# Kernel optimization log

Hardware: AMD Instinct MI355X
Metric: run time of the kernel (lower is better)

Reference implementation:

```python
import jax, jax.numpy as jnp
import numpy as np

N = 100000
E = 3200000
F_IN = 256
D_OUT = 128


def setup_inputs() -> dict:
    key = jax.random.key(0)
    ks = jax.random.split(key, 12)
    x = jax.random.normal(ks[0], (N, F_IN), dtype=jnp.float32)
    adj_val = jax.random.uniform(ks[1], (E,), dtype=jnp.float32)
    edge_row = jnp.sort(jax.random.randint(ks[2], (E,), 0, N))
    edge_col = jax.random.randint(ks[3], (E,), 0, N)
    # learned params (glorot-ish scaling)
    W1 = jax.random.normal(ks[4], (F_IN, D_OUT), dtype=jnp.float32) * (1.0 / np.sqrt(F_IN))   # conv1d_1 (1x1, no bias)
    w2 = jax.random.normal(ks[5], (D_OUT, 1), dtype=jnp.float32) * (1.0 / np.sqrt(D_OUT))     # conv1d_2
    b2 = jnp.zeros((1,), dtype=jnp.float32)
    w3 = jax.random.normal(ks[6], (D_OUT, 1), dtype=jnp.float32) * (1.0 / np.sqrt(D_OUT))     # conv1d_3
    b3 = jnp.zeros((1,), dtype=jnp.float32)
    kernel = jax.random.normal(ks[7], (F_IN, D_OUT), dtype=jnp.float32) * (1.0 / np.sqrt(F_IN))
    bias = jax.random.normal(ks[8], (N, D_OUT), dtype=jnp.float32) * 0.02
    return {"x": x, "adj_val": adj_val, "W1": W1, "w2": w2, "b2": b2,
            "w3": w3, "b3": b3, "kernel": kernel, "bias": bias,
            "edge_row": edge_row, "edge_col": edge_col}


def reference(x, adj_val, W1, w2, b2, w3, b3, kernel, bias, edge_row, edge_col):
    # 1x1 conv projections (equivalent to per-node dense layers)
    mapped = x @ W1                                   # [N, D]
    sa1 = (mapped @ w2 + b2)[:, 0]                    # [N]
    sa2 = (mapped @ w3 + b3)[:, 0]                    # [N]
    # sparse*dense broadcast then sparse add: per edge (i,j):
    #   adj_val * sa1[i] + adj_val * sa2[j]
    e = adj_val * (sa1[edge_row] + sa2[edge_col])     # [E]
    e = jax.nn.leaky_relu(e, negative_slope=0.2)
    # sparse row-wise softmax over nonzero entries
    m = jax.ops.segment_max(e, edge_row, num_segments=N)        # [N]
    m = jnp.where(jnp.isfinite(m), m, 0.0)
    ex = jnp.exp(e - m[edge_row])                               # [E]
    denom = jax.ops.segment_sum(ex, edge_row, num_segments=N)   # [N]
    denom = jnp.where(denom > 0, denom, 1.0)
    att = ex / denom[edge_row]                                  # [E]
    # dense feature transform then SpMM aggregation
    value = x @ kernel                                          # [N, D_OUT]
    out = jax.ops.segment_sum(att[:, None] * value[edge_col], edge_row, num_segments=N)
    out = out + bias                                            # use_bias=True
    return out  # activation=None (linear), single head, 'average' reduction
```

## Files before the change

### kernel.cpp

```cpp
#include <hip/hip_runtime.h>
#include <math.h>

#define N_NODES 100000
#define N_EDGES 3200000
#define F_IN    256
#define D_OUT   128

typedef __attribute__((ext_vector_type(8))) short short8;
typedef __attribute__((ext_vector_type(4))) float f32x4;

__device__ __forceinline__ unsigned short f2bf(float f) {
    unsigned u = __float_as_uint(f);
    unsigned r = (u + 0x7FFFu + ((u >> 16) & 1u)) >> 16;
    return (unsigned short)r;
}

__device__ __forceinline__ float dot4(float4 a, float4 b) {
    return a.x * b.x + a.y * b.y + a.z * b.z + a.w * b.w;
}

__device__ __forceinline__ float sb(unsigned u, int k) {
    return (float)((int)(u << ((3 - k) * 8)) >> 24);
}

__global__ __launch_bounds__(128) void prep_kernel(
    const float* __restrict__ W1, const float* __restrict__ w2,
    const float* __restrict__ w3, const float* __restrict__ kern,
    float* __restrict__ v1, float* __restrict__ v2,
    unsigned short* __restrict__ kbT) {
    const int kk  = blockIdx.x;
    const int tid = threadIdx.x;
    kbT[(size_t)tid * F_IN + kk] = f2bf(kern[(size_t)kk * D_OUT + tid]);
    if (tid < 64) {
        const float* wr = W1 + (size_t)kk * D_OUT;
        float a = wr[tid], b = wr[tid + 64];
        float s1 = a * w2[tid] + b * w2[tid + 64];
        float s2 = a * w3[tid] + b * w3[tid + 64];
#pragma unroll
        for (int o = 32; o > 0; o >>= 1) {
            s1 += __shfl_xor(s1, o);
            s2 += __shfl_xor(s2, o);
        }
        if (tid == 0) { v1[kk] = s1; v2[kk] = s2; }
    }
}

__global__ void row_ptr_kernel(const int* __restrict__ edge_row,
                               int* __restrict__ row_ptr) {
    int r = blockIdx.x * blockDim.x + threadIdx.x;
    if (r > N_NODES) return;
    int lo = 0, hi = N_EDGES;
    while (lo < hi) {
        int mid = (lo + hi) >> 1;
        if (edge_row[mid] < r) lo = mid + 1; else hi = mid;
    }
    row_ptr[r] = lo;
}

__global__ __launch_bounds__(256) void gemm_sa_kernel(
    const float* __restrict__ x, const unsigned short* __restrict__ kbT,
    const float* __restrict__ v1, const float* __restrict__ v2,
    const float* __restrict__ b2p, const float* __restrict__ b3p,
    signed char* __restrict__ valq, float* __restrict__ scale,
    float* __restrict__ sa1, float* __restrict__ sa2) {
    const int wid = blockIdx.x * 4 + (threadIdx.x >> 6);
    const int m_base = wid * 32;
    if (m_base >= N_NODES) return;
    const int lane = threadIdx.x & 63;
    const int r = lane & 15;
    const int q = lane >> 4;

    const float4* x0 = (const float4*)(x + (size_t)(m_base + r) * F_IN + q * 8);
    const float4* x1 = (const float4*)(x + (size_t)(m_base + 16 + r) * F_IN + q * 8);

    f32x4 acc[2][8];
#pragma unroll
    for (int t = 0; t < 2; ++t)
#pragma unroll
        for (int nt = 0; nt < 8; ++nt) acc[t][nt] = (f32x4)(0.f);
    float s1a = 0.f, s1b = 0.f, s2a = 0.f, s2b = 0.f;

#pragma unroll 2
    for (int s = 0; s < 8; ++s) {
        float4 p00 = x0[s * 8];
        float4 p01 = x0[s * 8 + 1];
        float4 p10 = x1[s * 8];
        float4 p11 = x1[s * 8 + 1];
        const float4* vp1 = (const float4*)(v1 + s * 32 + q * 8);
        const float4* vp2 = (const float4*)(v2 + s * 32 + q * 8);
        float4 va = vp1[0], vb = vp1[1], vc = vp2[0], vd = vp2[1];
        s1a += dot4(p00, va) + dot4(p01, vb);
        s2a += dot4(p00, vc) + dot4(p01, vd);
        s1b += dot4(p10, va) + dot4(p11, vb);
        s2b += dot4(p10, vc) + dot4(p11, vd);

        short8 a0, a1;
        a0[0] = (short)f2bf(p00.x); a0[1] = (short)f2bf(p00.y);
        a0[2] = (short)f2bf(p00.z); a0[3] = (short)f2bf(p00.w);
        a0[4] = (short)f2bf(p01.x); a0[5] = (short)f2bf(p01.y);
        a0[6] = (short)f2bf(p01.z); a0[7] = (short)f2bf(p01.w);
        a1[0] = (short)f2bf(p10.x); a1[1] = (short)f2bf(p10.y);
        a1[2] = (short)f2bf(p10.z); a1[3] = (short)f2bf(p10.w);
        a1[4] = (short)f2bf(p11.x); a1[5] = (short)f2bf(p11.y);
        a1[6] = (short)f2bf(p11.z); a1[7] = (short)f2bf(p11.w);

#pragma unroll
        for (int nt = 0; nt < 8; ++nt) {
            const short8 b = *(const short8*)(kbT + (size_t)(nt * 16 + r) * F_IN
                                              + s * 32 + q * 8);
            acc[0][nt] = __builtin_amdgcn_mfma_f32_16x16x32_bf16(a0, b, acc[0][nt], 0, 0, 0);
            acc[1][nt] = __builtin_amdgcn_mfma_f32_16x16x32_bf16(a1, b, acc[1][nt], 0, 0, 0);
        }
    }

    s1a += __shfl_xor(s1a, 16); s1a += __shfl_xor(s1a, 32);
    s1b += __shfl_xor(s1b, 16); s1b += __shfl_xor(s1b, 32);
    s2a += __shfl_xor(s2a, 16); s2a += __shfl_xor(s2a, 32);
    s2b += __shfl_xor(s2b, 16); s2b += __shfl_xor(s2b, 32);
    if (q == 0) {
        float bb2 = b2p[0], bb3 = b3p[0];
        sa1[m_base + r]      = s1a + bb2;
        sa1[m_base + 16 + r] = s1b + bb2;
        sa2[m_base + r]      = s2a + bb3;
        sa2[m_base + 16 + r] = s2b + bb3;
    }

#pragma unroll
    for (int t = 0; t < 2; ++t)
#pragma unroll
        for (int reg = 0; reg < 4; ++reg) {
            float m = 0.f;
#pragma unroll
            for (int nt = 0; nt < 8; ++nt) m = fmaxf(m, fabsf(acc[t][nt][reg]));
            m = fmaxf(m, __shfl_xor(m, 1));
            m = fmaxf(m, __shfl_xor(m, 2));
            m = fmaxf(m, __shfl_xor(m, 4));
            m = fmaxf(m, __shfl_xor(m, 8));
            const int row = m_base + t * 16 + q * 4 + reg;
            const float inv = m > 0.f ? 127.f / m : 0.f;
            if (r == 0) scale[row] = m * (1.f / 127.f);
#pragma unroll
            for (int nt = 0; nt < 8; ++nt) {
                int iq = (int)rintf(acc[t][nt][reg] * inv);
                valq[(size_t)row * D_OUT + nt * 16 + r] = (signed char)iq;
            }
        }
}

__global__ __launch_bounds__(256) void attn_agg_kernel(
    const int* __restrict__ row_ptr, const int* __restrict__ edge_col,
    const float* __restrict__ adj, const float* __restrict__ sa1,
    const float* __restrict__ sa2, const signed char* __restrict__ valq,
    const float* __restrict__ scale, const float* __restrict__ bias,
    float* __restrict__ out) {
    const int lane = threadIdx.x & 63;
    int row = blockIdx.x * 4 + (threadIdx.x >> 6);
    if (row >= N_NODES) return;
    row = __builtin_amdgcn_readfirstlane(row);

    const int s   = row_ptr[row];
    const int cnt = row_ptr[row + 1] - s;
    const float sa1r = sa1[row];

    const int g = lane >> 4;
    const int r = lane & 15;
    float acc[8];
#pragma unroll
    for (int j = 0; j < 8; ++j) acc[j] = 0.f;
    float sum = 0.f;

    const int full = cnt & ~3;
    int i = 0;
#pragma unroll 4
    for (; i < full; i += 4) {
        int e = s + i + g;
        int c = edge_col[e];
        float t = adj[e] * (sa1r + sa2[c]);
        t = t > 0.f ? t : 0.2f * t;
        float ex = __expf(t);
        float sc = scale[c];
        uint2 p = *(const uint2*)(valq + (size_t)c * D_OUT + r * 8);
        sum += ex;
        float w = ex * sc;
        acc[0] += w * sb(p.x, 0); acc[1] += w * sb(p.x, 1);
        acc[2] += w * sb(p.x, 2); acc[3] += w * sb(p.x, 3);
        acc[4] += w * sb(p.y, 0); acc[5] += w * sb(p.y, 1);
        acc[6] += w * sb(p.y, 2); acc[7] += w * sb(p.y, 3);
    }
    if (i + g < cnt) {
        int e = s + i + g;
        int c = edge_col[e];
        float t = adj[e] * (sa1r + sa2[c]);
        t = t > 0.f ? t : 0.2f * t;
        float ex = __expf(t);
        float sc = scale[c];
        uint2 p = *(const uint2*)(valq + (size_t)c * D_OUT + r * 8);
        sum += ex;
        float w = ex * sc;
        acc[0] += w * sb(p.x, 0); acc[1] += w * sb(p.x, 1);
        acc[2] += w * sb(p.x, 2); acc[3] += w * sb(p.x, 3);
        acc[4] += w * sb(p.y, 0); acc[5] += w * sb(p.y, 1);
        acc[6] += w * sb(p.y, 2); acc[7] += w * sb(p.y, 3);
    }

#pragma unroll
    for (int o = 16; o < 64; o <<= 1) {
        sum += __shfl_xor(sum, o);
#pragma unroll
        for (int j = 0; j < 8; ++j) acc[j] += __shfl_xor(acc[j], o);
    }
    const float inv = sum > 0.f ? 1.f / sum : 1.f;

    if (g == 0) {
        const float4* bp = (const float4*)(bias + (size_t)row * D_OUT + r * 8);
        float4 b0 = bp[0], b1 = bp[1];
        float4 r0, r1;
        r0.x = acc[0] * inv + b0.x; r0.y = acc[1] * inv + b0.y;
        r0.z = acc[2] * inv + b0.z; r0.w = acc[3] * inv + b0.w;
        r1.x = acc[4] * inv + b1.x; r1.y = acc[5] * inv + b1.y;
        r1.z = acc[6] * inv + b1.z; r1.w = acc[7] * inv + b1.w;
        float4* op = (float4*)(out + (size_t)row * D_OUT + r * 8);
        op[0] = r0; op[1] = r1;
    }
}

extern "C" void kernel_launch(void* const* d_in, const int* in_sizes, int n_in,
                              void* d_out, int out_size, void* d_ws,
                              size_t ws_size, hipStream_t stream) {
    const float* x        = (const float*)d_in[0];
    const float* adj      = (const float*)d_in[1];
    const float* W1       = (const float*)d_in[2];
    const float* w2       = (const float*)d_in[3];
    const float* b2       = (const float*)d_in[4];
    const float* w3       = (const float*)d_in[5];
    const float* b3       = (const float*)d_in[6];
    const float* kern     = (const float*)d_in[7];
    const float* bias     = (const float*)d_in[8];
    const int*   edge_row = (const int*)d_in[9];
    const int*   edge_col = (const int*)d_in[10];
    float* out = (float*)d_out;

    signed char* valq = (signed char*)d_ws;
    float* scale = (float*)(valq + (size_t)N_NODES * D_OUT);
    float* sa1 = scale + N_NODES;
    float* sa2 = sa1 + N_NODES;
    int*   row_ptr = (int*)(sa2 + N_NODES);
    float* v1 = (float*)(row_ptr + N_NODES + 4);
    float* v2 = v1 + F_IN;
    unsigned short* kbT = (unsigned short*)(v2 + F_IN);

    hipLaunchKernelGGL(prep_kernel, dim3(256), dim3(128), 0, stream,
                       W1, w2, w3, kern, v1, v2, kbT);
    hipLaunchKernelGGL(row_ptr_kernel, dim3((N_NODES + 1 + 255) / 256),
                       dim3(256), 0, stream, edge_row, row_ptr);
    hipLaunchKernelGGL(gemm_sa_kernel, dim3((N_NODES / 32 + 3) / 4), dim3(256),
                       0, stream, x, kbT, v1, v2, b2, b3, valq, scale, sa1,
                       sa2);
    hipLaunchKernelGGL(attn_agg_kernel, dim3(N_NODES / 4), dim3(256), 0,
                       stream, row_ptr, edge_col, adj, sa1, sa2, valq, scale,
                       bias, out);
}
```

Before: 370.2 us.

## Compute edge attention weights once per lane and broadcast via shuffles

The aggregation kernel now gives each of the 64 lanes its own edge for a chunk of up to 64 edges. Each lane computes the score, exp and scale-weighted factor for that edge, and the column index and weight are broadcast with shuffles to the 16-lane groups that gather the int8 value rows. Before, every lane in a 16-lane group recomputed the same edge score, loads and exp. Separately, streaming reads of x, edge_col, adj and bias and the output writes use nontemporal load and store hints, and the exp sum needs a full 64-lane reduction.

```diff
diff --git a/kernel.cpp b/kernel.cpp
--- a/kernel.cpp
+++ b/kernel.cpp
@@ -15,7 +15,7 @@
     return (unsigned short)r;
 }
 
-__device__ __forceinline__ float dot4(float4 a, float4 b) {
+__device__ __forceinline__ float dot4(f32x4 a, f32x4 b) {
     return a.x * b.x + a.y * b.y + a.z * b.z + a.w * b.w;
 }
 
@@ -70,8 +70,8 @@
     const int r = lane & 15;
     const int q = lane >> 4;
 
-    const float4* x0 = (const float4*)(x + (size_t)(m_base + r) * F_IN + q * 8);
-    const float4* x1 = (const float4*)(x + (size_t)(m_base + 16 + r) * F_IN + q * 8);
+    const f32x4* x0 = (const f32x4*)(x + (size_t)(m_base + r) * F_IN + q * 8);
+    const f32x4* x1 = (const f32x4*)(x + (size_t)(m_base + 16 + r) * F_IN + q * 8);
 
     f32x4 acc[2][8];
 #pragma unroll
@@ -82,13 +82,13 @@
 
 #pragma unroll 2
     for (int s = 0; s < 8; ++s) {
-        float4 p00 = x0[s * 8];
-        float4 p01 = x0[s * 8 + 1];
-        float4 p10 = x1[s * 8];
-        float4 p11 = x1[s * 8 + 1];
-        const float4* vp1 = (const float4*)(v1 + s * 32 + q * 8);
-        const float4* vp2 = (const float4*)(v2 + s * 32 + q * 8);
-        float4 va = vp1[0], vb = vp1[1], vc = vp2[0], vd = vp2[1];
+        f32x4 p00 = __builtin_nontemporal_load(x0 + s * 8);
+        f32x4 p01 = __builtin_nontemporal_load(x0 + s * 8 + 1);
+        f32x4 p10 = __builtin_nontemporal_load(x1 + s * 8);
+        f32x4 p11 = __builtin_nontemporal_load(x1 + s * 8 + 1);
+        const f32x4* vp1 = (const f32x4*)(v1 + s * 32 + q * 8);
+        const f32x4* vp2 = (const f32x4*)(v2 + s * 32 + q * 8);
+        f32x4 va = vp1[0], vb = vp1[1], vc = vp2[0], vd = vp2[1];
         s1a += dot4(p00, va) + dot4(p01, vb);
         s2a += dot4(p00, vc) + dot4(p01, vd);
         s1b += dot4(p10, va) + dot4(p11, vb);
@@ -164,45 +164,45 @@
 
     const int g = lane >> 4;
     const int r = lane & 15;
+    const signed char* vbase = valq + r * 8;
+
     float acc[8];
 #pragma unroll
     for (int j = 0; j < 8; ++j) acc[j] = 0.f;
     float sum = 0.f;
 
-    const int full = cnt & ~3;
-    int i = 0;
+    for (int base = 0; base < cnt; base += 64) {
+        const int n = min(64, cnt - base);
+
+        int c = 0;
+        float w = 0.f;
+        if (lane < n) {
+            const int e = s + base + lane;
+            c = __builtin_nontemporal_load(edge_col + e);
+            const float a = __builtin_nontemporal_load(adj + e);
+            float t = a * (sa1r + sa2[c]);
+            t = fmaxf(t, 0.2f * t);
+            const float ex = __expf(t);
+            sum += ex;
+            w = ex * scale[c];
+        }
+
 #pragma unroll 4
-    for (; i < full; i += 4) {
-        int e = s + i + g;
-        int c = edge_col[e];
-        float t = adj[e] * (sa1r + sa2[c]);
-        t = t > 0.f ? t : 0.2f * t;
-        float ex = __expf(t);
-        float sc = scale[c];
-        uint2 p = *(const uint2*)(valq + (size_t)c * D_OUT + r * 8);
-        sum += ex;
-        float w = ex * sc;
-        acc[0] += w * sb(p.x, 0); acc[1] += w * sb(p.x, 1);
-        acc[2] += w * sb(p.x, 2); acc[3] += w * sb(p.x, 3);
-        acc[4] += w * sb(p.y, 0); acc[5] += w * sb(p.y, 1);
-        acc[6] += w * sb(p.y, 2); acc[7] += w * sb(p.y, 3);
-    }
-    if (i + g < cnt) {
-        int e = s + i + g;
-        int c = edge_col[e];
-        float t = adj[e] * (sa1r + sa2[c]);
-        t = t > 0.f ? t : 0.2f * t;
-        float ex = __expf(t);
-        float sc = scale[c];
-        uint2 p = *(const uint2*)(valq + (size_t)c * D_OUT + r * 8);
-        sum += ex;
-        float w = ex * sc;
-        acc[0] += w * sb(p.x, 0); acc[1] += w * sb(p.x, 1);
-        acc[2] += w * sb(p.x, 2); acc[3] += w * sb(p.x, 3);
-        acc[4] += w * sb(p.y, 0); acc[5] += w * sb(p.y, 1);
-        acc[6] += w * sb(p.y, 2); acc[7] += w * sb(p.y, 3);
-    }
-
+        for (int i = 0; i < n; i += 4) {
+            const int   cc = __shfl(c, i + g);
+            const float ww = __shfl(w, i + g);
+            const uint2 p = *(const uint2*)(vbase + (size_t)cc * D_OUT);
+            acc[0] += ww * sb(p.x, 0); acc[1] += ww * sb(p.x, 1);
+            acc[2] += ww * sb(p.x, 2); acc[3] += ww * sb(p.x, 3);
+            acc[4] += ww * sb(p.y, 0); acc[5] += ww * sb(p.y, 1);
+            acc[6] += ww * sb(p.y, 2); acc[7] += ww * sb(p.y, 3);
+        }
+    }
+
+    sum += __shfl_xor(sum, 1);
+    sum += __shfl_xor(sum, 2);
+    sum += __shfl_xor(sum, 4);
+    sum += __shfl_xor(sum, 8);
 #pragma unroll
     for (int o = 16; o < 64; o <<= 1) {
         sum += __shfl_xor(sum, o);
@@ -212,15 +212,17 @@
     const float inv = sum > 0.f ? 1.f / sum : 1.f;
 
     if (g == 0) {
-        const float4* bp = (const float4*)(bias + (size_t)row * D_OUT + r * 8);
-        float4 b0 = bp[0], b1 = bp[1];
-        float4 r0, r1;
+        const f32x4* bp = (const f32x4*)(bias + (size_t)row * D_OUT + r * 8);
+        f32x4 b0 = __builtin_nontemporal_load(bp);
+        f32x4 b1 = __builtin_nontemporal_load(bp + 1);
+        f32x4 r0, r1;
         r0.x = acc[0] * inv + b0.x; r0.y = acc[1] * inv + b0.y;
         r0.z = acc[2] * inv + b0.z; r0.w = acc[3] * inv + b0.w;
         r1.x = acc[4] * inv + b1.x; r1.y = acc[5] * inv + b1.y;
         r1.z = acc[6] * inv + b1.z; r1.w = acc[7] * inv + b1.w;
-        float4* op = (float4*)(out + (size_t)row * D_OUT + r * 8);
-        op[0] = r0; op[1] = r1;
+        f32x4* op = (f32x4*)(out + (size_t)row * D_OUT + r * 8);
+        __builtin_nontemporal_store(r0, op);
+        __builtin_nontemporal_store(r1, op + 1);
     }
 }
 
```

Measured after the change: 377.3 us. About the same (+1.9%).
